# Kernel optimization log

Measured on AMD Instinct MI355X. Metric: run time of the kernel, lower is better.

Reference implementation:

```python
import jax, jax.numpy as jnp
import numpy as np

B, L, H, E, R = 4, 512, 768, 10, 10

def setup_inputs() -> dict:
    key = jax.random.key(0)
    ks = jax.random.split(key, 7)
    s = 1.0 / np.sqrt(H)
    return {
        "h": jax.random.normal(ks[0], (B, L, H), dtype=jnp.float32),
        "W_proj": jax.random.normal(ks[1], (H, H), dtype=jnp.float32) * s,
        "b_proj": jax.random.normal(ks[2], (H,), dtype=jnp.float32) * s,
        "W_ent": jax.random.normal(ks[3], (E, H), dtype=jnp.float32) * s,
        "b_ent": jax.random.normal(ks[4], (E,), dtype=jnp.float32) * s,
        "W_bil": jax.random.normal(ks[5], (R, H, H), dtype=jnp.float32) * s,
        "b_bil": jax.random.normal(ks[6], (R,), dtype=jnp.float32) * s,
    }

def reference(h, W_proj, b_proj, W_ent, b_ent, W_bil, b_bil):
    # h: (B, L, H)
    h_proj = jax.nn.relu(jnp.einsum('blh,kh->blk', h, W_proj) + b_proj)  # Linear: x @ W^T + b
    ent_logits = jnp.einsum('blh,eh->ble', h_proj, W_ent) + b_ent        # (B, L, E)
    # nn.Bilinear on all (i, j) pairs: rel[b,i,j,r] = h_i^T W_r h_j + b_r.
    # Factored O(L^2*H*R + L*H^2*R) instead of materializing (B,L,L,H) pairs.
    t = jnp.einsum('rhk,bmk->brmh', W_bil, h_proj)                        # (B, R, L, H)
    rel_logits = jnp.einsum('blh,brmh->blmr', h_proj, t) + b_bil          # (B, L, L, R)
    return (ent_logits, rel_logits)
```

## Files before the change

kernel.cpp:

```cpp
#include <hip/hip_runtime.h>
#include <stdint.h>

#define Bdim 4
#define Ldim 512
#define Hdim 768
#define Edim 10
#define Rdim 10

typedef __attribute__((ext_vector_type(8))) short short8;
typedef __attribute__((ext_vector_type(4))) float floatx4;

__device__ __forceinline__ unsigned short f2bf(float x) {
    unsigned int u = __float_as_uint(x);
    unsigned int r = (u + 0x7fffu + ((u >> 16) & 1u)) >> 16;
    return (unsigned short)r;
}
__device__ __forceinline__ float bf2f(unsigned short u) {
    return __uint_as_float(((unsigned int)u) << 16);
}

#define GLOAD_LDS16(g, l)                                                      \
    __builtin_amdgcn_global_load_lds(                                          \
        (const __attribute__((address_space(1))) void*)(g),                    \
        (__attribute__((address_space(3))) void*)(l), 16, 0, 0)

#define WAITVM(n) asm volatile("s_waitcnt vmcnt(" #n ")" ::: "memory")

__global__ void k_cvt4(const float* __restrict__ s0, unsigned short* __restrict__ d0, int n0,
                       const float* __restrict__ s1, unsigned short* __restrict__ d1, int n1,
                       const float* __restrict__ s2, unsigned short* __restrict__ d2, int n2,
                       const float* __restrict__ s3, unsigned short* __restrict__ d3, int n3) {
    int total = n0 + n1 + n2 + n3;
    int i = blockIdx.x * blockDim.x + threadIdx.x;
    int stride = gridDim.x * blockDim.x;
    for (; i < total; i += stride) {
        const float* s; unsigned short* d; int j = i;
        if (j < n0) { s = s0; d = d0; }
        else { j -= n0;
            if (j < n1) { s = s1; d = d1; }
            else { j -= n1;
                if (j < n2) { s = s2; d = d2; }
                else { j -= n2; s = s3; d = d3; }
            }
        }
        float4 v = reinterpret_cast<const float4*>(s)[j];
        ushort4 o;
        o.x = f2bf(v.x); o.y = f2bf(v.y); o.z = f2bf(v.z); o.w = f2bf(v.w);
        reinterpret_cast<ushort4*>(d)[j] = o;
    }
}

__device__ __forceinline__ int xcd_swz(int bid, int nwg) {
    int cpx = nwg >> 3;
    return (bid & 7) * cpx + (bid >> 3);
}

__device__ __forceinline__ void gemm_bt_core64_db(
    const unsigned short* __restrict__ A, int lda,
    const unsigned short* __restrict__ Bm, int ldb,
    int K,
    unsigned short* lA, unsigned short* lB,
    floatx4 acc[4][4])
{
    const int tid  = threadIdx.x;
    const int lane = tid & 63;
    const int wave = tid >> 6;
    const int wr = wave >> 1;
    const int wc = wave & 1;

    const int srow   = tid >> 3;
    const int schunk = (tid & 7) ^ (srow & 7);
    const int skk    = schunk << 3;

    const int frow = lane & 15;
    const int fs   = lane >> 4;

    #pragma unroll
    for (int i = 0; i < 4; ++i) {
        GLOAD_LDS16(A  + (size_t)(srow + 32 * i) * lda + skk,
                    lA + (tid + 256 * i) * 8);
        GLOAD_LDS16(Bm + (size_t)(srow + 32 * i) * ldb + skk,
                    lB + (tid + 256 * i) * 8);
    }
    __syncthreads();

    const int nt = K >> 6;
    int buf = 0;
    for (int kt = 0; kt < nt; ++kt) {
        if (kt + 1 < nt) {
            const int k0n = (kt + 1) << 6;
            unsigned short* dA = lA + (buf ^ 1) * 8192;
            unsigned short* dB = lB + (buf ^ 1) * 8192;
            #pragma unroll
            for (int i = 0; i < 4; ++i) {
                GLOAD_LDS16(A  + (size_t)(srow + 32 * i) * lda + k0n + skk,
                            dA + (tid + 256 * i) * 8);
                GLOAD_LDS16(Bm + (size_t)(srow + 32 * i) * ldb + k0n + skk,
                            dB + (tid + 256 * i) * 8);
            }
        }
        const unsigned short* sA = lA + buf * 8192;
        const unsigned short* sB = lB + buf * 8192;
        #pragma unroll
        for (int h = 0; h < 2; ++h) {
            short8 af[4], bfr[4];
            #pragma unroll
            for (int mi = 0; mi < 4; ++mi) {
                int row  = wr * 64 + mi * 16 + frow;
                int slot = (fs + 4 * h) ^ (row & 7);
                af[mi] = *reinterpret_cast<const short8*>(sA + row * 64 + slot * 8);
            }
            #pragma unroll
            for (int ni = 0; ni < 4; ++ni) {
                int row  = wc * 64 + ni * 16 + frow;
                int slot = (fs + 4 * h) ^ (row & 7);
                bfr[ni] = *reinterpret_cast<const short8*>(sB + row * 64 + slot * 8);
            }
            #pragma unroll
            for (int mi = 0; mi < 4; ++mi)
                #pragma unroll
                for (int ni = 0; ni < 4; ++ni)
                    acc[mi][ni] = __builtin_amdgcn_mfma_f32_16x16x32_bf16(
                        af[mi], bfr[ni], acc[mi][ni], 0, 0, 0);
        }
        __syncthreads();
        buf ^= 1;
    }
}

__device__ __forceinline__ void gemm_bt_core256_cnt(
    const unsigned short* __restrict__ A, int lda,
    const unsigned short* __restrict__ Bm, int ldb,
    unsigned short* lA, unsigned short* lB,
    floatx4 acc[8][4])
{
    const int tid  = threadIdx.x;
    const int lane = tid & 63;
    const int wave = tid >> 6;
    const int wr = wave >> 2;
    const int wc = wave & 3;

    const int srow   = tid >> 3;
    const int schunk = (tid & 7) ^ (srow & 7);
    const int skk    = schunk << 3;

    const int frow = lane & 15;
    const int fs   = lane >> 4;

    #define STAGE256(t, buf)                                                   \
        do {                                                                   \
            const int k0s = (t) << 6;                                          \
            unsigned short* dA = lA + (buf) * 16384;                           \
            unsigned short* dB = lB + (buf) * 16384;                           \
            _Pragma("unroll")                                                  \
            for (int i = 0; i < 4; ++i) {                                      \
                GLOAD_LDS16(A  + (size_t)(srow + 64 * i) * lda + k0s + skk,    \
                            dA + (tid + 512 * i) * 8);                         \
                GLOAD_LDS16(Bm + (size_t)(srow + 64 * i) * ldb + k0s + skk,    \
                            dB + (tid + 512 * i) * 8);                         \
            }                                                                  \
        } while (0)

    #define COMPUTE256(buf)                                                    \
        do {                                                                   \
            const unsigned short* sA = lA + (buf) * 16384;                     \
            const unsigned short* sB = lB + (buf) * 16384;                     \
            _Pragma("unroll")                                                  \
            for (int h = 0; h < 2; ++h) {                                      \
                short8 bfr[4];                                                 \
                _Pragma("unroll")                                              \
                for (int ni = 0; ni < 4; ++ni) {                               \
                    int row  = wc * 64 + ni * 16 + frow;                       \
                    int slot = (fs + 4 * h) ^ (row & 7);                       \
                    bfr[ni] = *reinterpret_cast<const short8*>(                \
                        sB + row * 64 + slot * 8);                             \
                }                                                              \
                _Pragma("unroll")                                              \
                for (int mi = 0; mi < 8; ++mi) {                               \
                    int row  = wr * 128 + mi * 16 + frow;                      \
                    int slot = (fs + 4 * h) ^ (row & 7);                       \
                    short8 af = *reinterpret_cast<const short8*>(              \
                        sA + row * 64 + slot * 8);                             \
                    _Pragma("unroll")                                          \
                    for (int ni = 0; ni < 4; ++ni)                             \
                        acc[mi][ni] = __builtin_amdgcn_mfma_f32_16x16x32_bf16( \
                            af, bfr[ni], acc[mi][ni], 0, 0, 0);                \
                }                                                              \
            }                                                                  \
        } while (0)

    const int NT = Hdim >> 6;

    STAGE256(0, 0);
    for (int kt = 0; kt < NT - 1; ++kt) {
        __builtin_amdgcn_s_barrier();
        STAGE256(kt + 1, (kt + 1) & 1);
        WAITVM(8);
        __builtin_amdgcn_s_barrier();
        __builtin_amdgcn_sched_barrier(0);
        COMPUTE256(kt & 1);
    }
    __builtin_amdgcn_s_barrier();
    WAITVM(0);
    __builtin_amdgcn_s_barrier();
    __builtin_amdgcn_sched_barrier(0);
    COMPUTE256((NT - 1) & 1);

    #undef STAGE256
    #undef COMPUTE256
}

__global__ __launch_bounds__(256) void k_gemm_proj(
    const unsigned short* __restrict__ hA,
    const unsigned short* __restrict__ Wp,
    const float* __restrict__ bproj,
    unsigned short* __restrict__ hp)
{
    __shared__ unsigned short lA[2 * 128 * 64];
    __shared__ unsigned short lB[2 * 128 * 64];
    int bid = xcd_swz(blockIdx.x + gridDim.x * blockIdx.y, gridDim.x * gridDim.y);
    const int m0 = (bid % gridDim.x) * 128;
    const int n0 = (bid / gridDim.x) * 128;
    floatx4 acc[4][4];
    #pragma unroll
    for (int i = 0; i < 4; ++i)
        #pragma unroll
        for (int j = 0; j < 4; ++j)
            acc[i][j] = (floatx4){0.f, 0.f, 0.f, 0.f};

    gemm_bt_core64_db(hA + (size_t)m0 * Hdim, Hdim,
                      Wp + (size_t)n0 * Hdim, Hdim, Hdim, lA, lB, acc);

    const int tid = threadIdx.x, lane = tid & 63, wave = tid >> 6;
    const int wr = wave >> 1, wc = wave & 1;
    const int cl = lane & 15, rh = (lane >> 4) * 4;
    #pragma unroll
    for (int mi = 0; mi < 4; ++mi)
        #pragma unroll
        for (int ni = 0; ni < 4; ++ni)
            #pragma unroll
            for (int j = 0; j < 4; ++j) {
                int r = m0 + wr * 64 + mi * 16 + rh + j;
                int c = n0 + wc * 64 + ni * 16 + cl;
                float v = acc[mi][ni][j] + bproj[c];
                hp[(size_t)r * Hdim + c] = f2bf(fmaxf(v, 0.0f));
            }
}

__global__ __launch_bounds__(512, 1) void k_gemm_t(
    const unsigned short* __restrict__ hp,
    const unsigned short* __restrict__ Wb,
    unsigned short* __restrict__ T)
{
    __shared__ unsigned short lA[2 * 256 * 64];
    __shared__ unsigned short lB[2 * 256 * 64];
    int bid = xcd_swz(blockIdx.x + gridDim.x * blockIdx.y, gridDim.x * gridDim.y);
    const int m0 = (bid % gridDim.x) * 256;
    const int n0 = (bid / gridDim.x) * 256;
    floatx4 acc[8][4];
    #pragma unroll
    for (int i = 0; i < 8; ++i)
        #pragma unroll
        for (int j = 0; j < 4; ++j)
            acc[i][j] = (floatx4){0.f, 0.f, 0.f, 0.f};

    gemm_bt_core256_cnt(hp + (size_t)m0 * Hdim, Hdim,
                        Wb + (size_t)n0 * Hdim, Hdim, lA, lB, acc);

    const int tid = threadIdx.x, lane = tid & 63, wave = tid >> 6;
    const int wr = wave >> 2, wc = wave & 3;
    const int cl = lane & 15, rh = (lane >> 4) * 4;
    #pragma unroll
    for (int mi = 0; mi < 8; ++mi)
        #pragma unroll
        for (int ni = 0; ni < 4; ++ni)
            #pragma unroll
            for (int j = 0; j < 4; ++j) {
                int r = m0 + wr * 128 + mi * 16 + rh + j;
                int c = n0 + wc * 64 + ni * 16 + cl;
                T[(size_t)r * (Rdim * Hdim) + c] = f2bf(acc[mi][ni][j]);
            }
}

__global__ __launch_bounds__(512, 1) void k_gemm_rel(
    const unsigned short* __restrict__ hp,
    const unsigned short* __restrict__ T,
    const float* __restrict__ bbil,
    float* __restrict__ rel)
{
    __shared__ unsigned short lA[2 * 256 * 64];
    __shared__ unsigned short lB[2 * 256 * 64];
    int bid = xcd_swz(blockIdx.x + gridDim.x * blockIdx.y, gridDim.x * gridDim.y);
    const int m0 = (bid % gridDim.x) * 256;
    const int n0 = (bid / gridDim.x) * 256;
    const int b  = m0 >> 9;
    floatx4 acc[8][4];
    #pragma unroll
    for (int i = 0; i < 8; ++i)
        #pragma unroll
        for (int j = 0; j < 4; ++j)
            acc[i][j] = (floatx4){0.f, 0.f, 0.f, 0.f};

    const unsigned short* Ab = hp + (size_t)m0 * Hdim;
    const unsigned short* Bb = T + (size_t)b * Ldim * (Rdim * Hdim) + (size_t)n0 * Hdim;
    gemm_bt_core256_cnt(Ab, Hdim, Bb, Hdim, lA, lB, acc);

    const int tid = threadIdx.x, lane = tid & 63, wave = tid >> 6;
    const int wr = wave >> 2, wc = wave & 3;
    const int cl = lane & 15, rh = (lane >> 4) * 4;
    #pragma unroll
    for (int mi = 0; mi < 8; ++mi)
        #pragma unroll
        for (int ni = 0; ni < 4; ++ni) {
            int n = n0 + wc * 64 + ni * 16 + cl;
            float bias = bbil[n % Rdim];
            #pragma unroll
            for (int j = 0; j < 4; ++j) {
                int grow = m0 + wr * 128 + mi * 16 + rh + j;
                rel[(size_t)grow * (Ldim * Rdim) + n] = acc[mi][ni][j] + bias;
            }
        }
}

__global__ __launch_bounds__(256) void k_ent(
    const unsigned short* __restrict__ hp,
    const unsigned short* __restrict__ We,
    const float* __restrict__ bent,
    float* __restrict__ out)
{
    const int gw = (blockIdx.x * blockDim.x + threadIdx.x) >> 6;
    const int lane = threadIdx.x & 63;
    if (gw >= Bdim * Ldim) return;
    const unsigned short* row = hp + (size_t)gw * Hdim;
    float hv[12];
    #pragma unroll
    for (int j = 0; j < 12; ++j) hv[j] = bf2f(row[lane + j * 64]);
    #pragma unroll
    for (int e = 0; e < Edim; ++e) {
        const unsigned short* wrow = We + e * Hdim;
        float s = 0.f;
        #pragma unroll
        for (int j = 0; j < 12; ++j) s += hv[j] * bf2f(wrow[lane + j * 64]);
        #pragma unroll
        for (int off = 32; off >= 1; off >>= 1) s += __shfl_xor(s, off);
        if (lane == 0) out[(size_t)gw * Edim + e] = s + bent[e];
    }
}

extern "C" void kernel_launch(void* const* d_in, const int* in_sizes, int n_in,
                              void* d_out, int out_size, void* d_ws, size_t ws_size,
                              hipStream_t stream)
{
    const float* h     = (const float*)d_in[0];
    const float* Wproj = (const float*)d_in[1];
    const float* bproj = (const float*)d_in[2];
    const float* Went  = (const float*)d_in[3];
    const float* bent  = (const float*)d_in[4];
    const float* Wbil  = (const float*)d_in[5];
    const float* bbil  = (const float*)d_in[6];

    float* out_ent = (float*)d_out;
    float* out_rel = (float*)d_out + (size_t)Bdim * Ldim * Edim;

    unsigned short* h_bf  = (unsigned short*)d_ws;
    unsigned short* Wp_bf = h_bf  + (size_t)2048 * Hdim;
    unsigned short* Wb_bf = Wp_bf + (size_t)Hdim * Hdim;
    unsigned short* We_bf = Wb_bf + (size_t)Rdim * Hdim * Hdim;
    unsigned short* hp_bf = We_bf + (size_t)Edim * Hdim;
    unsigned short* T_bf  = hp_bf + (size_t)2048 * Hdim;

    {
        int n0 = 2048 * Hdim / 4;
        int n1 = Hdim * Hdim / 4;
        int n2 = Rdim * Hdim * Hdim / 4;
        int n3 = Edim * Hdim / 4;
        k_cvt4<<<dim3(2048), 256, 0, stream>>>(h, h_bf, n0, Wproj, Wp_bf, n1,
                                               Wbil, Wb_bf, n2, Went, We_bf, n3);
    }

    k_gemm_proj<<<dim3(2048 / 128, Hdim / 128), 256, 0, stream>>>(h_bf, Wp_bf, bproj, hp_bf);

    k_ent<<<dim3((Bdim * Ldim * 64) / 256), 256, 0, stream>>>(hp_bf, We_bf, bent, out_ent);

    k_gemm_t<<<dim3(2048 / 256, (Rdim * Hdim) / 256), 512, 0, stream>>>(hp_bf, Wb_bf, T_bf);

    k_gemm_rel<<<dim3(2048 / 256, (Ldim * Rdim) / 256), 512, 0, stream>>>(hp_bf, T_bf, bbil, out_rel);
}
```

Before: 174.4 us.

## Fuse fp32-to-bf16 conversion into projection GEMM and merge small kernels

The projection GEMM now reads fp32 h and W_proj directly, converts them to bf16 in registers and writes them to LDS. This removes the separate conversion pass over those tensors. The remaining weight conversion runs in extra blocks of the same launch, and the entity-logit computation runs as extra blocks inside the relation GEMM launch, cutting five launches to three. The trade-off is that the projection GEMM loses async global-to-LDS double buffering, using register prefetch with a single LDS buffer and two barriers per k-tile.

```diff
diff --git a/kernel.cpp b/kernel.cpp
--- a/kernel.cpp
+++ b/kernel.cpp
@@ -26,106 +26,9 @@
 
 #define WAITVM(n) asm volatile("s_waitcnt vmcnt(" #n ")" ::: "memory")
 
-__global__ void k_cvt4(const float* __restrict__ s0, unsigned short* __restrict__ d0, int n0,
-                       const float* __restrict__ s1, unsigned short* __restrict__ d1, int n1,
-                       const float* __restrict__ s2, unsigned short* __restrict__ d2, int n2,
-                       const float* __restrict__ s3, unsigned short* __restrict__ d3, int n3) {
-    int total = n0 + n1 + n2 + n3;
-    int i = blockIdx.x * blockDim.x + threadIdx.x;
-    int stride = gridDim.x * blockDim.x;
-    for (; i < total; i += stride) {
-        const float* s; unsigned short* d; int j = i;
-        if (j < n0) { s = s0; d = d0; }
-        else { j -= n0;
-            if (j < n1) { s = s1; d = d1; }
-            else { j -= n1;
-                if (j < n2) { s = s2; d = d2; }
-                else { j -= n2; s = s3; d = d3; }
-            }
-        }
-        float4 v = reinterpret_cast<const float4*>(s)[j];
-        ushort4 o;
-        o.x = f2bf(v.x); o.y = f2bf(v.y); o.z = f2bf(v.z); o.w = f2bf(v.w);
-        reinterpret_cast<ushort4*>(d)[j] = o;
-    }
-}
-
 __device__ __forceinline__ int xcd_swz(int bid, int nwg) {
     int cpx = nwg >> 3;
     return (bid & 7) * cpx + (bid >> 3);
-}
-
-__device__ __forceinline__ void gemm_bt_core64_db(
-    const unsigned short* __restrict__ A, int lda,
-    const unsigned short* __restrict__ Bm, int ldb,
-    int K,
-    unsigned short* lA, unsigned short* lB,
-    floatx4 acc[4][4])
-{
-    const int tid  = threadIdx.x;
-    const int lane = tid & 63;
-    const int wave = tid >> 6;
-    const int wr = wave >> 1;
-    const int wc = wave & 1;
-
-    const int srow   = tid >> 3;
-    const int schunk = (tid & 7) ^ (srow & 7);
-    const int skk    = schunk << 3;
-
-    const int frow = lane & 15;
-    const int fs   = lane >> 4;
-
-    #pragma unroll
-    for (int i = 0; i < 4; ++i) {
-        GLOAD_LDS16(A  + (size_t)(srow + 32 * i) * lda + skk,
-                    lA + (tid + 256 * i) * 8);
-        GLOAD_LDS16(Bm + (size_t)(srow + 32 * i) * ldb + skk,
-                    lB + (tid + 256 * i) * 8);
-    }
-    __syncthreads();
-
-    const int nt = K >> 6;
-    int buf = 0;
-    for (int kt = 0; kt < nt; ++kt) {
-        if (kt + 1 < nt) {
-            const int k0n = (kt + 1) << 6;
-            unsigned short* dA = lA + (buf ^ 1) * 8192;
-            unsigned short* dB = lB + (buf ^ 1) * 8192;
-            #pragma unroll
-            for (int i = 0; i < 4; ++i) {
-                GLOAD_LDS16(A  + (size_t)(srow + 32 * i) * lda + k0n + skk,
-                            dA + (tid + 256 * i) * 8);
-                GLOAD_LDS16(Bm + (size_t)(srow + 32 * i) * ldb + k0n + skk,
-                            dB + (tid + 256 * i) * 8);
-            }
-        }
-        const unsigned short* sA = lA + buf * 8192;
-        const unsigned short* sB = lB + buf * 8192;
-        #pragma unroll
-        for (int h = 0; h < 2; ++h) {
-            short8 af[4], bfr[4];
-            #pragma unroll
-            for (int mi = 0; mi < 4; ++mi) {
-                int row  = wr * 64 + mi * 16 + frow;
-                int slot = (fs + 4 * h) ^ (row & 7);
-                af[mi] = *reinterpret_cast<const short8*>(sA + row * 64 + slot * 8);
-            }
-            #pragma unroll
-            for (int ni = 0; ni < 4; ++ni) {
-                int row  = wc * 64 + ni * 16 + frow;
-                int slot = (fs + 4 * h) ^ (row & 7);
-                bfr[ni] = *reinterpret_cast<const short8*>(sB + row * 64 + slot * 8);
-            }
-            #pragma unroll
-            for (int mi = 0; mi < 4; ++mi)
-                #pragma unroll
-                for (int ni = 0; ni < 4; ++ni)
-                    acc[mi][ni] = __builtin_amdgcn_mfma_f32_16x16x32_bf16(
-                        af[mi], bfr[ni], acc[mi][ni], 0, 0, 0);
-        }
-        __syncthreads();
-        buf ^= 1;
-    }
 }
 
 __device__ __forceinline__ void gemm_bt_core256_cnt(
@@ -210,17 +113,46 @@
     #undef COMPUTE256
 }
 
-__global__ __launch_bounds__(256) void k_gemm_proj(
-    const unsigned short* __restrict__ hA,
-    const unsigned short* __restrict__ Wp,
+__global__ __launch_bounds__(256) void k_prep(
+    const float* __restrict__ h,   const float* __restrict__ Wp,
     const float* __restrict__ bproj,
-    unsigned short* __restrict__ hp)
-{
-    __shared__ unsigned short lA[2 * 128 * 64];
-    __shared__ unsigned short lB[2 * 128 * 64];
-    int bid = xcd_swz(blockIdx.x + gridDim.x * blockIdx.y, gridDim.x * gridDim.y);
-    const int m0 = (bid % gridDim.x) * 128;
-    const int n0 = (bid / gridDim.x) * 128;
+    const float* __restrict__ Wbil, const float* __restrict__ We,
+    unsigned short* __restrict__ hp,
+    unsigned short* __restrict__ Wb_bf, unsigned short* __restrict__ We_bf)
+{
+    __shared__ unsigned short lA[128 * 64];
+    __shared__ unsigned short lB[128 * 64];
+    const int tid = threadIdx.x;
+
+    if (blockIdx.x >= 96) {
+        const int n2 = Rdim * Hdim * Hdim / 4;
+        const int n3 = Edim * Hdim / 4;
+        int i = (blockIdx.x - 96) * 256 + tid;
+        const int stride = (gridDim.x - 96) * 256;
+        for (; i < n2 + n3; i += stride) {
+            const float* s; unsigned short* d; int j = i;
+            if (j < n2) { s = Wbil; d = Wb_bf; }
+            else { j -= n2; s = We; d = We_bf; }
+            float4 v = reinterpret_cast<const float4*>(s)[j];
+            ushort4 o;
+            o.x = f2bf(v.x); o.y = f2bf(v.y); o.z = f2bf(v.z); o.w = f2bf(v.w);
+            reinterpret_cast<ushort4*>(d)[j] = o;
+        }
+        return;
+    }
+
+    int bid = xcd_swz(blockIdx.x, 96);
+    const int m0 = (bid % 16) * 128;
+    const int n0 = (bid / 16) * 128;
+    const float* Asrc = h  + (size_t)m0 * Hdim;
+    const float* Bsrc = Wp + (size_t)n0 * Hdim;
+
+    const int lane = tid & 63;
+    const int wave = tid >> 6;
+    const int wr = wave >> 1, wc = wave & 1;
+    const int frow = lane & 15;
+    const int fs   = lane >> 4;
+
     floatx4 acc[4][4];
     #pragma unroll
     for (int i = 0; i < 4; ++i)
@@ -228,11 +160,69 @@
         for (int j = 0; j < 4; ++j)
             acc[i][j] = (floatx4){0.f, 0.f, 0.f, 0.f};
 
-    gemm_bt_core64_db(hA + (size_t)m0 * Hdim, Hdim,
-                      Wp + (size_t)n0 * Hdim, Hdim, Hdim, lA, lB, acc);
-
-    const int tid = threadIdx.x, lane = tid & 63, wave = tid >> 6;
-    const int wr = wave >> 1, wc = wave & 1;
+    float4 ra[4][2], rb[4][2];
+    #define LOADREGS(k0s)                                                      \
+        _Pragma("unroll")                                                      \
+        for (int i = 0; i < 4; ++i) {                                          \
+            int q = tid + 256 * i, row = q >> 3, pchk = q & 7;                 \
+            int lchk = pchk ^ (row & 7);                                       \
+            const float* sa = Asrc + (size_t)row * Hdim + (k0s) + lchk * 8;    \
+            const float* sb = Bsrc + (size_t)row * Hdim + (k0s) + lchk * 8;    \
+            ra[i][0] = *reinterpret_cast<const float4*>(sa);                   \
+            ra[i][1] = *reinterpret_cast<const float4*>(sa + 4);               \
+            rb[i][0] = *reinterpret_cast<const float4*>(sb);                   \
+            rb[i][1] = *reinterpret_cast<const float4*>(sb + 4);               \
+        }
+
+    LOADREGS(0);
+    const int NT = Hdim >> 6;
+    for (int kt = 0; kt < NT; ++kt) {
+        short8 pa[4], pb[4];
+        #pragma unroll
+        for (int i = 0; i < 4; ++i) {
+            pa[i][0] = f2bf(ra[i][0].x); pa[i][1] = f2bf(ra[i][0].y);
+            pa[i][2] = f2bf(ra[i][0].z); pa[i][3] = f2bf(ra[i][0].w);
+            pa[i][4] = f2bf(ra[i][1].x); pa[i][5] = f2bf(ra[i][1].y);
+            pa[i][6] = f2bf(ra[i][1].z); pa[i][7] = f2bf(ra[i][1].w);
+            pb[i][0] = f2bf(rb[i][0].x); pb[i][1] = f2bf(rb[i][0].y);
+            pb[i][2] = f2bf(rb[i][0].z); pb[i][3] = f2bf(rb[i][0].w);
+            pb[i][4] = f2bf(rb[i][1].x); pb[i][5] = f2bf(rb[i][1].y);
+            pb[i][6] = f2bf(rb[i][1].z); pb[i][7] = f2bf(rb[i][1].w);
+        }
+        __syncthreads();
+        #pragma unroll
+        for (int i = 0; i < 4; ++i) {
+            int q = tid + 256 * i, row = q >> 3, pchk = q & 7;
+            *reinterpret_cast<short8*>(lA + row * 64 + pchk * 8) = pa[i];
+            *reinterpret_cast<short8*>(lB + row * 64 + pchk * 8) = pb[i];
+        }
+        if (kt + 1 < NT) LOADREGS((kt + 1) << 6);
+        __syncthreads();
+        #pragma unroll
+        for (int hh = 0; hh < 2; ++hh) {
+            short8 af[4], bfr[4];
+            #pragma unroll
+            for (int mi = 0; mi < 4; ++mi) {
+                int row  = wr * 64 + mi * 16 + frow;
+                int slot = (fs + 4 * hh) ^ (row & 7);
+                af[mi] = *reinterpret_cast<const short8*>(lA + row * 64 + slot * 8);
+            }
+            #pragma unroll
+            for (int ni = 0; ni < 4; ++ni) {
+                int row  = wc * 64 + ni * 16 + frow;
+                int slot = (fs + 4 * hh) ^ (row & 7);
+                bfr[ni] = *reinterpret_cast<const short8*>(lB + row * 64 + slot * 8);
+            }
+            #pragma unroll
+            for (int mi = 0; mi < 4; ++mi)
+                #pragma unroll
+                for (int ni = 0; ni < 4; ++ni)
+                    acc[mi][ni] = __builtin_amdgcn_mfma_f32_16x16x32_bf16(
+                        af[mi], bfr[ni], acc[mi][ni], 0, 0, 0);
+        }
+    }
+    #undef LOADREGS
+
     const int cl = lane & 15, rh = (lane >> 4) * 4;
     #pragma unroll
     for (int mi = 0; mi < 4; ++mi)
@@ -282,17 +272,44 @@
             }
 }
 
-__global__ __launch_bounds__(512, 1) void k_gemm_rel(
+__global__ __launch_bounds__(512, 1) void k_rel_ent(
     const unsigned short* __restrict__ hp,
     const unsigned short* __restrict__ T,
     const float* __restrict__ bbil,
-    float* __restrict__ rel)
+    float* __restrict__ rel,
+    const unsigned short* __restrict__ We,
+    const float* __restrict__ bent,
+    float* __restrict__ out_ent)
 {
     __shared__ unsigned short lA[2 * 256 * 64];
     __shared__ unsigned short lB[2 * 256 * 64];
-    int bid = xcd_swz(blockIdx.x + gridDim.x * blockIdx.y, gridDim.x * gridDim.y);
-    const int m0 = (bid % gridDim.x) * 256;
-    const int n0 = (bid / gridDim.x) * 256;
+    const int tid = threadIdx.x, lane = tid & 63, wave = tid >> 6;
+
+    if (blockIdx.x >= 160) {
+        const int e = blockIdx.x - 160;
+        const int base = (e * 8 + wave) * 8;
+        for (int rr = 0; rr < 8; ++rr) {
+            const unsigned short* row = hp + (size_t)(base + rr) * Hdim;
+            float hv[12];
+            #pragma unroll
+            for (int j = 0; j < 12; ++j) hv[j] = bf2f(row[lane + j * 64]);
+            #pragma unroll
+            for (int ee = 0; ee < Edim; ++ee) {
+                const unsigned short* wrow = We + ee * Hdim;
+                float s = 0.f;
+                #pragma unroll
+                for (int j = 0; j < 12; ++j) s += hv[j] * bf2f(wrow[lane + j * 64]);
+                #pragma unroll
+                for (int off = 32; off >= 1; off >>= 1) s += __shfl_xor(s, off);
+                if (lane == 0) out_ent[(size_t)(base + rr) * Edim + ee] = s + bent[ee];
+            }
+        }
+        return;
+    }
+
+    int bid = xcd_swz(blockIdx.x, 160);
+    const int m0 = (bid & 7) * 256;
+    const int n0 = (bid >> 3) * 256;
     const int b  = m0 >> 9;
     floatx4 acc[8][4];
     #pragma unroll
@@ -305,7 +322,6 @@
     const unsigned short* Bb = T + (size_t)b * Ldim * (Rdim * Hdim) + (size_t)n0 * Hdim;
     gemm_bt_core256_cnt(Ab, Hdim, Bb, Hdim, lA, lB, acc);
 
-    const int tid = threadIdx.x, lane = tid & 63, wave = tid >> 6;
     const int wr = wave >> 2, wc = wave & 3;
     const int cl = lane & 15, rh = (lane >> 4) * 4;
     #pragma unroll
@@ -320,31 +336,6 @@
                 rel[(size_t)grow * (Ldim * Rdim) + n] = acc[mi][ni][j] + bias;
             }
         }
-}
-
-__global__ __launch_bounds__(256) void k_ent(
-    const unsigned short* __restrict__ hp,
-    const unsigned short* __restrict__ We,
-    const float* __restrict__ bent,
-    float* __restrict__ out)
-{
-    const int gw = (blockIdx.x * blockDim.x + threadIdx.x) >> 6;
-    const int lane = threadIdx.x & 63;
-    if (gw >= Bdim * Ldim) return;
-    const unsigned short* row = hp + (size_t)gw * Hdim;
-    float hv[12];
-    #pragma unroll
-    for (int j = 0; j < 12; ++j) hv[j] = bf2f(row[lane + j * 64]);
-    #pragma unroll
-    for (int e = 0; e < Edim; ++e) {
-        const unsigned short* wrow = We + e * Hdim;
-        float s = 0.f;
-        #pragma unroll
-        for (int j = 0; j < 12; ++j) s += hv[j] * bf2f(wrow[lane + j * 64]);
-        #pragma unroll
-        for (int off = 32; off >= 1; off >>= 1) s += __shfl_xor(s, off);
-        if (lane == 0) out[(size_t)gw * Edim + e] = s + bent[e];
-    }
 }
 
 extern "C" void kernel_launch(void* const* d_in, const int* in_sizes, int n_in,
@@ -362,27 +353,16 @@
     float* out_ent = (float*)d_out;
     float* out_rel = (float*)d_out + (size_t)Bdim * Ldim * Edim;
 
-    unsigned short* h_bf  = (unsigned short*)d_ws;
-    unsigned short* Wp_bf = h_bf  + (size_t)2048 * Hdim;
-    unsigned short* Wb_bf = Wp_bf + (size_t)Hdim * Hdim;
+    unsigned short* Wb_bf = (unsigned short*)d_ws;
     unsigned short* We_bf = Wb_bf + (size_t)Rdim * Hdim * Hdim;
     unsigned short* hp_bf = We_bf + (size_t)Edim * Hdim;
     unsigned short* T_bf  = hp_bf + (size_t)2048 * Hdim;
 
-    {
-        int n0 = 2048 * Hdim / 4;
-        int n1 = Hdim * Hdim / 4;
-        int n2 = Rdim * Hdim * Hdim / 4;
-        int n3 = Edim * Hdim / 4;
-        k_cvt4<<<dim3(2048), 256, 0, stream>>>(h, h_bf, n0, Wproj, Wp_bf, n1,
-                                               Wbil, Wb_bf, n2, Went, We_bf, n3);
-    }
-
-    k_gemm_proj<<<dim3(2048 / 128, Hdim / 128), 256, 0, stream>>>(h_bf, Wp_bf, bproj, hp_bf);
-
-    k_ent<<<dim3((Bdim * Ldim * 64) / 256), 256, 0, stream>>>(hp_bf, We_bf, bent, out_ent);
+    k_prep<<<dim3(1120), 256, 0, stream>>>(h, Wproj, bproj, Wbil, Went,
+                                           hp_bf, Wb_bf, We_bf);
 
     k_gemm_t<<<dim3(2048 / 256, (Rdim * Hdim) / 256), 512, 0, stream>>>(hp_bf, Wb_bf, T_bf);
 
-    k_gemm_rel<<<dim3(2048 / 256, (Ldim * Rdim) / 256), 512, 0, stream>>>(hp_bf, T_bf, bbil, out_rel);
-}
+    k_rel_ent<<<dim3(192), 512, 0, stream>>>(hp_bf, T_bf, bbil, out_rel,
+                                             We_bf, bent, out_ent);
+}
```

New measurement: 169.4 us. 2.9% less time.
